# Optimization experiments

Hardware: AMD Instinct MI355X
Metric: run time of the kernel (lower is better)

Reference implementation:

```python
import jax, jax.numpy as jnp
import numpy as np

B, N, D, C, K = 16, 1024, 64, 64, 20
EPS = 1e-3  # keras BatchNormalization default epsilon


def _bn(x, g, b, mu, v):
    return (x - mu) * jax.lax.rsqrt(v + EPS) * g + b


def setup_inputs() -> dict:
    key = jax.random.key(0)
    ks = jax.random.split(key, 6)
    return {
        "feats": jax.random.normal(ks[0], (B, N, D), dtype=jnp.float32),
        "adj": jax.random.uniform(ks[1], (B, N, N), dtype=jnp.float32),
        "w1": jax.random.normal(ks[2], (2 * D, C), dtype=jnp.float32) * 0.05,
        "b1": jax.random.normal(ks[3], (C,), dtype=jnp.float32) * 0.05,
        "g1": jnp.ones((C,), jnp.float32),
        "be1": jnp.zeros((C,), jnp.float32),
        "mu1": jnp.zeros((C,), jnp.float32),
        "v1": jnp.ones((C,), jnp.float32),
        "w2": jax.random.normal(ks[4], (C, C), dtype=jnp.float32) * 0.05,
        "b2": jax.random.normal(ks[5], (C,), dtype=jnp.float32) * 0.05,
        "g2": jnp.ones((C,), jnp.float32),
        "be2": jnp.zeros((C,), jnp.float32),
        "mu2": jnp.zeros((C,), jnp.float32),
        "v2": jnp.ones((C,), jnp.float32),
        "k": K,
    }


def reference(feats, adj, w1, b1, g1, be1, mu1, v1, w2, b2, g2, be2, mu2, v2, k):
    # weighted distance matrix from feature channel 0
    f0 = feats[:, :, 0]                                   # (B,N)
    fdiff = jnp.abs(f0[:, None, :] - f0[:, :, None])       # |f[j]-f[i]| at (b,i,j)
    a = adj * fdiff                                        # (B,N,N)
    # KNN: top_k of negated distance
    _, nn_idx = jax.lax.top_k(-a, k)                       # (B,N,k)
    # edge feature gather
    knn_fts = jax.vmap(lambda f, idx: f[idx])(feats, nn_idx)          # (B,N,k,D)
    center = jnp.broadcast_to(feats[:, :, None, :], knn_fts.shape)    # (B,N,k,D)
    edge = jnp.concatenate([center, knn_fts - center], axis=-1)       # (B,N,k,2D)
    # two fused 1x1 conv + BN + ReLU
    x = jax.nn.relu(_bn(jnp.einsum('bnkd,dc->bnkc', edge, w1) + b1, g1, be1, mu1, v1))
    x = jax.nn.relu(_bn(jnp.einsum('bnkc,ce->bnke', x, w2) + b2, g2, be2, mu2, v2))
    # mean over neighbors
    return jnp.mean(x, axis=2)                             # (B,N,C)
```

## Files before the change

### kernel.cpp

```cpp
#include <hip/hip_runtime.h>
#include <float.h>
#include <math.h>

#define NN 1024
#define DD 64
#define CC 64
#define KK 20
#define EPSL 1e-3f

typedef __attribute__((ext_vector_type(8))) short short8;
typedef __attribute__((ext_vector_type(4))) float f32x4;

__device__ __forceinline__ unsigned short f2bf(float f) {
    unsigned u = __float_as_uint(f);
    return (unsigned short)((u + 0x7fffu + ((u >> 16) & 1u)) >> 16);
}
__device__ __forceinline__ float bf2f(unsigned short h) {
    return __uint_as_float((unsigned)h << 16);
}

__global__ __launch_bounds__(256) void k0_prep(
        const float* __restrict__ w1, const float* __restrict__ w2,
        const float* __restrict__ feats, const float* __restrict__ b1,
        const float* __restrict__ g1, const float* __restrict__ be1,
        const float* __restrict__ mu1, const float* __restrict__ v1,
        unsigned short* __restrict__ b1t, unsigned short* __restrict__ w2t,
        float* __restrict__ bb, float* __restrict__ f0c) {
    int t = blockIdx.x * 256 + threadIdx.x;
    if (t < 8192) {
        int n = t >> 6, k = t & 63;
        float val;
        if (n < 64) {
            float s = g1[n] * rsqrtf(v1[n] + EPSL);
            val = (w1[k * CC + n] - w1[(k + DD) * CC + n]) * s;
        } else {
            int c = n - 64;
            float s = g1[c] * rsqrtf(v1[c] + EPSL);
            val = w1[(k + DD) * CC + c] * s;
        }
        b1t[t] = f2bf(val);
    } else if (t < 12288) {
        int i = t - 8192;
        int n = i >> 6, k = i & 63;
        w2t[i] = f2bf(w2[k * CC + n]);
    } else if (t < 12352) {
        int c = t - 12288;
        float s = g1[c] * rsqrtf(v1[c] + EPSL);
        bb[c] = b1[c] * s + be1[c] - mu1[c] * s;
    } else if (t < 28736) {
        int u = t - 12352;
        f0c[u] = feats[(size_t)u * DD];
    }
}

__global__ __launch_bounds__(256) void k1_mfma(
        const float* __restrict__ feats, const unsigned short* __restrict__ b1t,
        const float* __restrict__ bb,
        float* __restrict__ cterm, float* __restrict__ nterm) {
    int lane = threadIdx.x & 63, w = threadIdx.x >> 6;
    int col = lane & 15, quad = lane >> 4;
    int m0 = blockIdx.x * 64;

    short8 bfr[2][2];
#pragma unroll
    for (int nt = 0; nt < 2; ++nt)
#pragma unroll
        for (int ks = 0; ks < 2; ++ks)
            bfr[nt][ks] = *(const short8*)(b1t + (w * 32 + nt * 16 + col) * 64 + ks * 32 + quad * 8);

    float bbv[2] = {0.f, 0.f};
    if (w < 2) {
        bbv[0] = bb[w * 32 + col];
        bbv[1] = bb[w * 32 + 16 + col];
    }

    f32x4 acc[4][2];
#pragma unroll
    for (int mt = 0; mt < 4; ++mt)
#pragma unroll
        for (int nt = 0; nt < 2; ++nt) acc[mt][nt] = (f32x4)(0.f);

#pragma unroll
    for (int mt = 0; mt < 4; ++mt) {
        const float* fr = feats + (size_t)(m0 + mt * 16 + col) * DD;
#pragma unroll
        for (int ks = 0; ks < 2; ++ks) {
            float4 p0 = *(const float4*)(fr + ks * 32 + quad * 8);
            float4 p1 = *(const float4*)(fr + ks * 32 + quad * 8 + 4);
            float f[8] = {p0.x, p0.y, p0.z, p0.w, p1.x, p1.y, p1.z, p1.w};
            short8 ah, al;
#pragma unroll
            for (int i = 0; i < 8; ++i) {
                unsigned short h = f2bf(f[i]);
                ah[i] = (short)h;
                al[i] = (short)f2bf(f[i] - bf2f(h));
            }
#pragma unroll
            for (int nt = 0; nt < 2; ++nt) {
                acc[mt][nt] = __builtin_amdgcn_mfma_f32_16x16x32_bf16(ah, bfr[nt][ks], acc[mt][nt], 0, 0, 0);
                acc[mt][nt] = __builtin_amdgcn_mfma_f32_16x16x32_bf16(al, bfr[nt][ks], acc[mt][nt], 0, 0, 0);
            }
        }
    }

#pragma unroll
    for (int mt = 0; mt < 4; ++mt)
#pragma unroll
        for (int nt = 0; nt < 2; ++nt) {
            int n = w * 32 + nt * 16 + col;
#pragma unroll
            for (int r = 0; r < 4; ++r) {
                int m = m0 + mt * 16 + quad * 4 + r;
                float v = acc[mt][nt][r];
                if (w < 2) cterm[(size_t)m * CC + n] = v + bbv[nt];
                else       nterm[(size_t)m * CC + (n - 64)] = v;
            }
        }
}

__global__ __launch_bounds__(256) void k2_topk(const float* __restrict__ adj,
                                               const float* __restrict__ f0c,
                                               int* __restrict__ nnidx) {
    __shared__ unsigned long long keybuf[4][64];
    int lane = threadIdx.x & 63;
    int w    = threadIdx.x >> 6;
    int row  = blockIdx.x * 4 + w;
    int b    = row >> 10;
    const float4* arow = (const float4*)(adj + (size_t)row * NN);
    const float4* frow = (const float4*)(f0c + (size_t)b * NN);
    float f0i = f0c[row];
    unsigned vu[16];
#pragma unroll
    for (int tv = 0; tv < 4; ++tv) {
        float4 av = arow[64 * tv + lane];
        float4 fv = frow[64 * tv + lane];
        vu[tv * 4 + 0] = __float_as_uint(av.x * fabsf(fv.x - f0i));
        vu[tv * 4 + 1] = __float_as_uint(av.y * fabsf(fv.y - f0i));
        vu[tv * 4 + 2] = __float_as_uint(av.z * fabsf(fv.z - f0i));
        vu[tv * 4 + 3] = __float_as_uint(av.w * fabsf(fv.w - f0i));
    }
    unsigned x = vu[0];
#pragma unroll
    for (int t = 1; t < 16; ++t) x = (vu[t] < x) ? vu[t] : x;
#pragma unroll
    for (int k = 2; k <= 64; k <<= 1) {
#pragma unroll
        for (int j = k >> 1; j > 0; j >>= 1) {
            unsigned o = __shfl_xor(x, j);
            bool keepmin = (((lane & j) == 0) == ((lane & k) == 0));
            unsigned mn = (o < x) ? o : x;
            unsigned mx = (o < x) ? x : o;
            x = keepmin ? mn : mx;
        }
    }
    unsigned T = __shfl(x, 19);
    int cnt = 0;
#pragma unroll
    for (int t = 0; t < 16; ++t) cnt += (vu[t] <= T) ? 1 : 0;
    int inc = cnt;
#pragma unroll
    for (int off = 1; off < 64; off <<= 1) {
        int o = __shfl_up(inc, off);
        if (lane >= off) inc += o;
    }
    int total = __shfl(inc, 63);
    int* outp = nnidx + (size_t)row * KK;

    if (total <= 64) {
        int pos = inc - cnt;
#pragma unroll
        for (int t = 0; t < 16; ++t) {
            if (vu[t] <= T) {
                int j = 256 * (t >> 2) + 4 * lane + (t & 3);
                keybuf[w][pos] = ((unsigned long long)vu[t] << 32) | (unsigned)j;
                pos++;
            }
        }
        unsigned long long key = (lane < total) ? keybuf[w][lane] : ~0ull;
        unsigned y = (unsigned)(key >> 32);
#pragma unroll
        for (int k = 2; k <= 64; k <<= 1) {
#pragma unroll
            for (int j = k >> 1; j > 0; j >>= 1) {
                unsigned o = __shfl_xor(y, j);
                bool keepmin = (((lane & j) == 0) == ((lane & k) == 0));
                unsigned mn = (o < y) ? o : y;
                unsigned mx = (o < y) ? y : o;
                y = keepmin ? mn : mx;
            }
        }
        unsigned Tstar = __shfl(y, 19);
        bool fl = (lane < total) && ((unsigned)(key >> 32) <= Tstar);
        unsigned long long msk = __ballot(fl);
        int p = __popcll(msk & ((1ull << lane) - 1ull));
        if (fl && p < KK) outp[p] = (int)(unsigned)key;
    } else {
        for (int r = 0; r < KK; ++r) {
            unsigned bv = vu[0];
            int bt = 0;
#pragma unroll
            for (int t = 1; t < 16; ++t) {
                if (vu[t] < bv) { bv = vu[t]; bt = t; }
            }
            int bj = 256 * (bt >> 2) + 4 * lane + (bt & 3);
            unsigned wv = bv;
            int wi = bj;
#pragma unroll
            for (int m = 1; m < 64; m <<= 1) {
                unsigned ov = __shfl_xor(wv, m);
                int oi = __shfl_xor(wi, m);
                if (ov < wv || (ov == wv && oi < wi)) { wv = ov; wi = oi; }
            }
            if (lane == 0) outp[r] = wi;
            if (((wi >> 2) & 63) == lane) {
                int s = ((wi >> 8) << 2) | (wi & 3);
#pragma unroll
                for (int t = 0; t < 16; ++t) {
                    if (t == s) vu[t] = 0xFFFFFFFFu;
                }
            }
        }
    }
}

__global__ __launch_bounds__(256, 3) void k3_mfma(
        const float* __restrict__ cterm, const float* __restrict__ nterm,
        const int* __restrict__ nnidx, const unsigned short* __restrict__ w2t,
        const float* __restrict__ b2,
        const float* __restrict__ g2, const float* __restrict__ be2,
        const float* __restrict__ mu2, const float* __restrict__ v2,
        float* __restrict__ out) {
    int lane = threadIdx.x & 63, w = threadIdx.x >> 6;
    int col = lane & 15, quad = lane >> 4;
    int wid = blockIdx.x * 4 + w;
    int u0 = wid * 4;
    int b  = u0 >> 10;

    short8 bfr[4][2];
#pragma unroll
    for (int nt = 0; nt < 4; ++nt)
#pragma unroll
        for (int ks = 0; ks < 2; ++ks)
            bfr[nt][ks] = *(const short8*)(w2t + (nt * 16 + col) * 64 + ks * 32 + quad * 8);

    float s2v[4], sh2v[4];
#pragma unroll
    for (int nt = 0; nt < 4; ++nt) {
        int c = nt * 16 + col;
        float s2 = g2[c] * rsqrtf(v2[c] + EPSL);
        s2v[nt]  = s2;
        sh2v[nt] = (b2[c] - mu2[c]) * s2 + be2[c];
    }

    f32x4 acc[5][4];
#pragma unroll
    for (int mt = 0; mt < 5; ++mt)
#pragma unroll
        for (int nt = 0; nt < 4; ++nt) acc[mt][nt] = (f32x4)(0.f);

    const int* ibase = nnidx + (size_t)u0 * KK;
#pragma unroll
    for (int mt = 0; mt < 5; ++mt) {
        int row = mt * 16 + col;
        int g   = (row * 205) >> 12;
        int j   = ibase[row];
        const float* np = nterm + (size_t)(b * NN + j) * CC;
        const float* cp = cterm + (size_t)(u0 + g) * CC;
        short8 afr[2];
#pragma unroll
        for (int ks = 0; ks < 2; ++ks) {
            int ch = ks * 32 + quad * 8;
            float4 n0 = *(const float4*)(np + ch);
            float4 n1 = *(const float4*)(np + ch + 4);
            float4 c0 = *(const float4*)(cp + ch);
            float4 c1 = *(const float4*)(cp + ch + 4);
            float h[8];
            h[0] = fmaxf(c0.x + n0.x, 0.f); h[1] = fmaxf(c0.y + n0.y, 0.f);
            h[2] = fmaxf(c0.z + n0.z, 0.f); h[3] = fmaxf(c0.w + n0.w, 0.f);
            h[4] = fmaxf(c1.x + n1.x, 0.f); h[5] = fmaxf(c1.y + n1.y, 0.f);
            h[6] = fmaxf(c1.z + n1.z, 0.f); h[7] = fmaxf(c1.w + n1.w, 0.f);
#pragma unroll
            for (int i = 0; i < 8; ++i) afr[ks][i] = (short)f2bf(h[i]);
        }
#pragma unroll
        for (int ks = 0; ks < 2; ++ks)
#pragma unroll
            for (int nt = 0; nt < 4; ++nt)
                acc[mt][nt] = __builtin_amdgcn_mfma_f32_16x16x32_bf16(afr[ks], bfr[nt][ks], acc[mt][nt], 0, 0, 0);
    }

    float us0[4] = {0,0,0,0}, us1[4] = {0,0,0,0}, us2[4] = {0,0,0,0}, us3[4] = {0,0,0,0};
#pragma unroll
    for (int mt = 0; mt < 5; ++mt)
#pragma unroll
        for (int nt = 0; nt < 4; ++nt) {
            float qs = 0.f;
#pragma unroll
            for (int r = 0; r < 4; ++r)
                qs += fmaxf(acc[mt][nt][r] * s2v[nt] + sh2v[nt], 0.f);
            if (mt == 0) us0[nt] += qs;
            else if (mt == 4) us3[nt] += qs;
            else if (mt == 1) { float t = (quad >= 1) ? qs : 0.f; us1[nt] += t; us0[nt] += qs - t; }
            else if (mt == 2) { float t = (quad >= 2) ? qs : 0.f; us2[nt] += t; us1[nt] += qs - t; }
            else              { float t = (quad >= 3) ? qs : 0.f; us3[nt] += t; us2[nt] += qs - t; }
        }
#pragma unroll
    for (int nt = 0; nt < 4; ++nt) {
        us0[nt] += __shfl_xor(us0[nt], 16); us0[nt] += __shfl_xor(us0[nt], 32);
        us1[nt] += __shfl_xor(us1[nt], 16); us1[nt] += __shfl_xor(us1[nt], 32);
        us2[nt] += __shfl_xor(us2[nt], 16); us2[nt] += __shfl_xor(us2[nt], 32);
        us3[nt] += __shfl_xor(us3[nt], 16); us3[nt] += __shfl_xor(us3[nt], 32);
    }
#pragma unroll
    for (int nt = 0; nt < 4; ++nt) {
        float v = (quad == 0) ? us0[nt] : (quad == 1) ? us1[nt] : (quad == 2) ? us2[nt] : us3[nt];
        out[(size_t)(u0 + quad) * CC + nt * 16 + col] = v * 0.05f;
    }
}

extern "C" void kernel_launch(void* const* d_in, const int* in_sizes, int n_in,
                              void* d_out, int out_size, void* d_ws, size_t ws_size,
                              hipStream_t stream) {
    const float* feats = (const float*)d_in[0];
    const float* adj   = (const float*)d_in[1];
    const float* w1    = (const float*)d_in[2];
    const float* b1    = (const float*)d_in[3];
    const float* g1    = (const float*)d_in[4];
    const float* be1   = (const float*)d_in[5];
    const float* mu1   = (const float*)d_in[6];
    const float* v1    = (const float*)d_in[7];
    const float* w2    = (const float*)d_in[8];
    const float* b2    = (const float*)d_in[9];
    const float* g2    = (const float*)d_in[10];
    const float* be2   = (const float*)d_in[11];
    const float* mu2   = (const float*)d_in[12];
    const float* v2    = (const float*)d_in[13];
    float* out = (float*)d_out;

    char* ws = (char*)d_ws;
    float*          cterm = (float*)(ws);
    float*          nterm = (float*)(ws + 4u * 1024 * 1024);
    float*          f0c   = (float*)(ws + 8u * 1024 * 1024);
    int*            nnidx = (int*)  (ws + 8u * 1024 * 1024 + 64u * 1024);
    unsigned short* b1t   = (unsigned short*)(ws + 10u * 1024 * 1024);
    unsigned short* w2t   = (unsigned short*)(ws + 10u * 1024 * 1024 + 16u * 1024);
    float*          bb    = (float*)(ws + 10u * 1024 * 1024 + 24u * 1024);

    k0_prep<<<113, 256, 0, stream>>>(w1, w2, feats, b1, g1, be1, mu1, v1,
                                     b1t, w2t, bb, f0c);
    k1_mfma<<<256, 256, 0, stream>>>(feats, b1t, bb, cterm, nterm);
    k2_topk<<<4096, 256, 0, stream>>>(adj, f0c, nnidx);
    k3_mfma<<<1024, 256, 0, stream>>>(cterm, nterm, nnidx, w2t, b2,
                                      g2, be2, mu2, v2, out);
}
```

Measured before the change: 152.8 us.

## Store layer-1 center/neighbor terms in bf16 and split k1 into smaller blocks

The intermediate cterm/nterm tensors are now written as bf16 instead of fp32, which halves the bytes k1 writes and the bytes k3 gathers per neighbor. k3 reads them with short8 loads and preloads all five neighbor indices up front. k1 now covers 16 rows per block across 1024 blocks instead of 64 rows across 256 blocks, for more parallelism. The cost is extra rounding in the layer-1 pre-activation, which is already rounded to bf16 before the second MFMA.

```diff
diff --git a/kernel.cpp b/kernel.cpp
--- a/kernel.cpp
+++ b/kernel.cpp
@@ -56,66 +56,60 @@
 __global__ __launch_bounds__(256) void k1_mfma(
         const float* __restrict__ feats, const unsigned short* __restrict__ b1t,
         const float* __restrict__ bb,
-        float* __restrict__ cterm, float* __restrict__ nterm) {
+        unsigned short* __restrict__ cterm, unsigned short* __restrict__ nterm) {
     int lane = threadIdx.x & 63, w = threadIdx.x >> 6;
     int col = lane & 15, quad = lane >> 4;
-    int m0 = blockIdx.x * 64;
+    int m0 = blockIdx.x * 16;
+    int nb = w * 32;
 
     short8 bfr[2][2];
 #pragma unroll
     for (int nt = 0; nt < 2; ++nt)
 #pragma unroll
         for (int ks = 0; ks < 2; ++ks)
-            bfr[nt][ks] = *(const short8*)(b1t + (w * 32 + nt * 16 + col) * 64 + ks * 32 + quad * 8);
+            bfr[nt][ks] = *(const short8*)(b1t + (nb + nt * 16 + col) * 64 + ks * 32 + quad * 8);
 
     float bbv[2] = {0.f, 0.f};
     if (w < 2) {
-        bbv[0] = bb[w * 32 + col];
-        bbv[1] = bb[w * 32 + 16 + col];
-    }
-
-    f32x4 acc[4][2];
-#pragma unroll
-    for (int mt = 0; mt < 4; ++mt)
-#pragma unroll
-        for (int nt = 0; nt < 2; ++nt) acc[mt][nt] = (f32x4)(0.f);
-
-#pragma unroll
-    for (int mt = 0; mt < 4; ++mt) {
-        const float* fr = feats + (size_t)(m0 + mt * 16 + col) * DD;
-#pragma unroll
-        for (int ks = 0; ks < 2; ++ks) {
-            float4 p0 = *(const float4*)(fr + ks * 32 + quad * 8);
-            float4 p1 = *(const float4*)(fr + ks * 32 + quad * 8 + 4);
-            float f[8] = {p0.x, p0.y, p0.z, p0.w, p1.x, p1.y, p1.z, p1.w};
-            short8 ah, al;
-#pragma unroll
-            for (int i = 0; i < 8; ++i) {
-                unsigned short h = f2bf(f[i]);
-                ah[i] = (short)h;
-                al[i] = (short)f2bf(f[i] - bf2f(h));
-            }
-#pragma unroll
-            for (int nt = 0; nt < 2; ++nt) {
-                acc[mt][nt] = __builtin_amdgcn_mfma_f32_16x16x32_bf16(ah, bfr[nt][ks], acc[mt][nt], 0, 0, 0);
-                acc[mt][nt] = __builtin_amdgcn_mfma_f32_16x16x32_bf16(al, bfr[nt][ks], acc[mt][nt], 0, 0, 0);
-            }
-        }
-    }
-
-#pragma unroll
-    for (int mt = 0; mt < 4; ++mt)
+        bbv[0] = bb[nb + col];
+        bbv[1] = bb[nb + 16 + col];
+    }
+
+    f32x4 acc[2];
+    acc[0] = (f32x4)(0.f);
+    acc[1] = (f32x4)(0.f);
+
+    const float* fr = feats + (size_t)(m0 + col) * DD;
+#pragma unroll
+    for (int ks = 0; ks < 2; ++ks) {
+        float4 p0 = *(const float4*)(fr + ks * 32 + quad * 8);
+        float4 p1 = *(const float4*)(fr + ks * 32 + quad * 8 + 4);
+        float f[8] = {p0.x, p0.y, p0.z, p0.w, p1.x, p1.y, p1.z, p1.w};
+        short8 ah, al;
+#pragma unroll
+        for (int i = 0; i < 8; ++i) {
+            unsigned short h = f2bf(f[i]);
+            ah[i] = (short)h;
+            al[i] = (short)f2bf(f[i] - bf2f(h));
+        }
 #pragma unroll
         for (int nt = 0; nt < 2; ++nt) {
-            int n = w * 32 + nt * 16 + col;
-#pragma unroll
-            for (int r = 0; r < 4; ++r) {
-                int m = m0 + mt * 16 + quad * 4 + r;
-                float v = acc[mt][nt][r];
-                if (w < 2) cterm[(size_t)m * CC + n] = v + bbv[nt];
-                else       nterm[(size_t)m * CC + (n - 64)] = v;
-            }
-        }
+            acc[nt] = __builtin_amdgcn_mfma_f32_16x16x32_bf16(ah, bfr[nt][ks], acc[nt], 0, 0, 0);
+            acc[nt] = __builtin_amdgcn_mfma_f32_16x16x32_bf16(al, bfr[nt][ks], acc[nt], 0, 0, 0);
+        }
+    }
+
+#pragma unroll
+    for (int nt = 0; nt < 2; ++nt) {
+        int n = nb + nt * 16 + col;
+#pragma unroll
+        for (int r = 0; r < 4; ++r) {
+            int m = m0 + quad * 4 + r;
+            unsigned short v = f2bf(acc[nt][r] + bbv[nt]);
+            if (w < 2) cterm[(size_t)m * CC + n] = v;
+            else       nterm[(size_t)m * CC + (n - 64)] = v;
+        }
+    }
 }
 
 __global__ __launch_bounds__(256) void k2_topk(const float* __restrict__ adj,
@@ -224,7 +218,7 @@
 }
 
 __global__ __launch_bounds__(256, 3) void k3_mfma(
-        const float* __restrict__ cterm, const float* __restrict__ nterm,
+        const unsigned short* __restrict__ cterm, const unsigned short* __restrict__ nterm,
         const int* __restrict__ nnidx, const unsigned short* __restrict__ w2t,
         const float* __restrict__ b2,
         const float* __restrict__ g2, const float* __restrict__ be2,
@@ -259,28 +253,27 @@
         for (int nt = 0; nt < 4; ++nt) acc[mt][nt] = (f32x4)(0.f);
 
     const int* ibase = nnidx + (size_t)u0 * KK;
+    int jrow[5];
+#pragma unroll
+    for (int mt = 0; mt < 5; ++mt) jrow[mt] = ibase[mt * 16 + col];
+
 #pragma unroll
     for (int mt = 0; mt < 5; ++mt) {
         int row = mt * 16 + col;
         int g   = (row * 205) >> 12;
-        int j   = ibase[row];
-        const float* np = nterm + (size_t)(b * NN + j) * CC;
-        const float* cp = cterm + (size_t)(u0 + g) * CC;
+        const unsigned short* np = nterm + (size_t)(b * NN + jrow[mt]) * CC;
+        const unsigned short* cp = cterm + (size_t)(u0 + g) * CC;
         short8 afr[2];
 #pragma unroll
         for (int ks = 0; ks < 2; ++ks) {
             int ch = ks * 32 + quad * 8;
-            float4 n0 = *(const float4*)(np + ch);
-            float4 n1 = *(const float4*)(np + ch + 4);
-            float4 c0 = *(const float4*)(cp + ch);
-            float4 c1 = *(const float4*)(cp + ch + 4);
-            float h[8];
-            h[0] = fmaxf(c0.x + n0.x, 0.f); h[1] = fmaxf(c0.y + n0.y, 0.f);
-            h[2] = fmaxf(c0.z + n0.z, 0.f); h[3] = fmaxf(c0.w + n0.w, 0.f);
-            h[4] = fmaxf(c1.x + n1.x, 0.f); h[5] = fmaxf(c1.y + n1.y, 0.f);
-            h[6] = fmaxf(c1.z + n1.z, 0.f); h[7] = fmaxf(c1.w + n1.w, 0.f);
-#pragma unroll
-            for (int i = 0; i < 8; ++i) afr[ks][i] = (short)f2bf(h[i]);
+            short8 nv = *(const short8*)(np + ch);
+            short8 cv = *(const short8*)(cp + ch);
+#pragma unroll
+            for (int i = 0; i < 8; ++i) {
+                float h = bf2f((unsigned short)cv[i]) + bf2f((unsigned short)nv[i]);
+                afr[ks][i] = (short)f2bf(fmaxf(h, 0.f));
+            }
         }
 #pragma unroll
         for (int ks = 0; ks < 2; ++ks)
@@ -338,17 +331,17 @@
     float* out = (float*)d_out;
 
     char* ws = (char*)d_ws;
-    float*          cterm = (float*)(ws);
-    float*          nterm = (float*)(ws + 4u * 1024 * 1024);
-    float*          f0c   = (float*)(ws + 8u * 1024 * 1024);
-    int*            nnidx = (int*)  (ws + 8u * 1024 * 1024 + 64u * 1024);
-    unsigned short* b1t   = (unsigned short*)(ws + 10u * 1024 * 1024);
-    unsigned short* w2t   = (unsigned short*)(ws + 10u * 1024 * 1024 + 16u * 1024);
-    float*          bb    = (float*)(ws + 10u * 1024 * 1024 + 24u * 1024);
+    unsigned short* cterm = (unsigned short*)(ws);
+    unsigned short* nterm = (unsigned short*)(ws + 2u * 1024 * 1024);
+    float*          f0c   = (float*)(ws + 4u * 1024 * 1024);
+    int*            nnidx = (int*)  (ws + 4u * 1024 * 1024 + 64u * 1024);
+    unsigned short* b1t   = (unsigned short*)(ws + 6u * 1024 * 1024);
+    unsigned short* w2t   = (unsigned short*)(ws + 6u * 1024 * 1024 + 16u * 1024);
+    float*          bb    = (float*)(ws + 6u * 1024 * 1024 + 24u * 1024);
 
     k0_prep<<<113, 256, 0, stream>>>(w1, w2, feats, b1, g1, be1, mu1, v1,
                                      b1t, w2t, bb, f0c);
-    k1_mfma<<<256, 256, 0, stream>>>(feats, b1t, bb, cterm, nterm);
+    k1_mfma<<<1024, 256, 0, stream>>>(feats, b1t, bb, cterm, nterm);
     k2_topk<<<4096, 256, 0, stream>>>(adj, f0c, nnidx);
     k3_mfma<<<1024, 256, 0, stream>>>(cterm, nterm, nnidx, w2t, b2,
                                       g2, be2, mu2, v2, out);
```

After: 148.1 us. 1.03x faster.
